# Kernel tuning notes

Measured on AMD Instinct MI355X. Metric: run time of the kernel, lower is better.

The kernel has to match this reference:

```python
import jax, jax.numpy as jnp
import numpy as np

N_NODES = 100000
N_EDGES = 1600000
IN_CH, OUT_CH = 6, 32


def _glorot(key, shape):
    fan_in, fan_out = shape[0], shape[1]
    lim = float(np.sqrt(6.0 / (fan_in + fan_out)))
    return jax.random.uniform(key, shape, jnp.float32, -lim, lim)


def setup_inputs() -> dict:
    key = jax.random.key(0)
    ks = jax.random.split(key, 16)
    x = jax.random.normal(ks[0], (N_NODES, IN_CH), jnp.float32)
    edge_tp = jax.random.randint(ks[1], (2, N_EDGES), 0, N_NODES, jnp.int32)
    edge_int = jax.random.randint(ks[2], (2, N_EDGES), 0, N_NODES, jnp.int32)
    return {
        'x': x, 'edge_tp': edge_tp, 'edge_int': edge_int,
        # block 1 (6 -> 32): self lin, per-edge-type message lins, residual proj
        'W_self1': _glorot(ks[3], (IN_CH, OUT_CH)), 'b1': jnp.zeros((OUT_CH,), jnp.float32),
        'W_tp1': _glorot(ks[4], (IN_CH, OUT_CH)), 'W_int1': _glorot(ks[5], (IN_CH, OUT_CH)),
        'W_res1': _glorot(ks[6], (IN_CH, OUT_CH)),
        # block 2 (32 -> 32): identity residual
        'W_self2': _glorot(ks[7], (OUT_CH, OUT_CH)), 'b2': jnp.zeros((OUT_CH,), jnp.float32),
        'W_tp2': _glorot(ks[8], (OUT_CH, OUT_CH)), 'W_int2': _glorot(ks[9], (OUT_CH, OUT_CH)),
        # instance decoder MLP
        'Wd1': _glorot(ks[10], (OUT_CH, OUT_CH)), 'bd1': jnp.zeros((OUT_CH,), jnp.float32),
        'Wd2': _glorot(ks[11], (OUT_CH, 1)), 'bd2': jnp.zeros((1,), jnp.float32),
    }


def _hetero_block(x, edge_tp, edge_int, W_self, b, W_tp, W_int, W_res):
    """One ResidualGeneralHeteroConvBlock: per-edge-type message passing
    ('temp_previous' -> sum-agg, 'intersects' -> mean-agg) + self transform +
    residual, then ReLU. x: [N, Cin]."""
    N = x.shape[0]
    # temp_previous: add reducer
    src, dst = edge_tp[0], edge_tp[1]
    m_tp = jax.ops.segment_sum(x[src] @ W_tp, dst, num_segments=N)  # [N, Cout]
    # intersects: mean reducer
    s2, d2 = edge_int[0], edge_int[1]
    m_sum = jax.ops.segment_sum(x[s2] @ W_int, d2, num_segments=N)
    cnt = jax.ops.segment_sum(jnp.ones(d2.shape, x.dtype), d2, num_segments=N)
    m_int = m_sum / jnp.maximum(cnt, 1.0)[:, None]
    res = x @ W_res if W_res is not None else x
    return jax.nn.relu(x @ W_self + b + m_tp + m_int + res)


def reference(x, edge_tp, edge_int,
              W_self1, b1, W_tp1, W_int1, W_res1,
              W_self2, b2, W_tp2, W_int2,
              Wd1, bd1, Wd2, bd2):
    h = _hetero_block(x, edge_tp, edge_int, W_self1, b1, W_tp1, W_int1, W_res1)
    h = _hetero_block(h, edge_tp, edge_int, W_self2, b2, W_tp2, W_int2, None)
    # instance decoder: Linear -> ReLU -> Linear -> sigmoid
    h = jax.nn.relu(h @ Wd1 + bd1)
    return jax.nn.sigmoid(h @ Wd2 + bd2)  # [N, 1]
```

## Files before the change

kernel.cpp:

```cpp
#include <hip/hip_runtime.h>
#include <hip/hip_bf16.h>
#include <math.h>

#define NN   100000
#define ICH  6
#define OCH  32
#define NBK  782
#define PBLK 256
#define CAPB 4736
#define CAPL 4800
#define GN   16

__device__ __forceinline__ float ldf(const void* p, long i, int f32) {
    return f32 ? ((const float*)p)[i]
               : __bfloat162float(((const __hip_bfloat16*)p)[i]);
}
__device__ __forceinline__ float lo16f(unsigned u) { return __uint_as_float(u << 16); }
__device__ __forceinline__ float hi16f(unsigned u) { return __uint_as_float(u & 0xFFFF0000u); }

__global__ __launch_bounds__(1024) void partAx_r14(
        const int* __restrict__ src_tp, const int* __restrict__ dst_tp,
        const int* __restrict__ src_int, const int* __restrict__ dst_int,
        int Etp, int E,
        const void* __restrict__ x, unsigned* __restrict__ xw,
        int* __restrict__ gcnt, unsigned* __restrict__ part,
        int* __restrict__ flagp) {
    __shared__ int lh[NBK];
    __shared__ int cur[NBK];
    __shared__ int weird;
    int t = threadIdx.x, blk = blockIdx.x;
    if (t == 0) weird = 0;
    for (int b = t; b < NBK; b += 1024) lh[b] = 0;
    __syncthreads();
    {
        const __hip_bfloat16* p = (const __hip_bfloat16*)x;
        int w = 0;
        for (int i = t; i < 4096; i += 1024) {
            float v = fabsf(__bfloat162float(p[i]));
            if (!(v <= 1000.0f) || (v > 0.0f && v < 1e-4f)) w++;
        }
        if (w) atomicAdd(&weird, w);
    }
    __syncthreads();
    int f32 = (weird > 500) ? 1 : 0;
    if (blk == 0 && t == 0) *flagp = f32;
    for (int w = blk * 1024 + t; w < NN * 4; w += PBLK * 1024) {
        int n = w >> 2, j = w & 3;
        int c0 = 2 * j, c1 = 2 * j + 1;
        __hip_bfloat16 v0 = (c0 < ICH) ? __float2bfloat16(ldf(x, (long)n * ICH + c0, f32))
                                       : __float2bfloat16(0.0f);
        __hip_bfloat16 v1 = (c1 < ICH) ? __float2bfloat16(ldf(x, (long)n * ICH + c1, f32))
                                       : __float2bfloat16(0.0f);
        xw[w] = (unsigned)__bfloat16_as_ushort(v0) |
                ((unsigned)__bfloat16_as_ushort(v1) << 16);
    }
    int CH = (E + PBLK - 1) / PBLK;
    int lo = blk * CH, hi = min(E, lo + CH);
    for (int e = lo + t; e < hi; e += 1024) {
        int bin = (e < Etp) ? dst_tp[e] : NN + dst_int[e - Etp];
        atomicAdd(&lh[bin >> 8], 1);
    }
    __syncthreads();
    for (int b = t; b < NBK; b += 1024) {
        int n = lh[b];
        int base = b * CAPB + (n ? atomicAdd(&gcnt[b], n) : gcnt[b]);
        cur[b] = base;
    }
    __syncthreads();
    for (int e = lo + t; e < hi; e += 1024) {
        int bin, src;
        if (e < Etp) { bin = dst_tp[e]; src = src_tp[e]; }
        else         { bin = NN + dst_int[e - Etp]; src = src_int[e - Etp]; }
        int pos = atomicAdd(&cur[bin >> 8], 1);
        part[pos] = ((unsigned)(bin & 255) << 24) | (unsigned)src;
    }
}

__global__ __launch_bounds__(256) void passB_r14(
        unsigned* __restrict__ partcsr, const int* __restrict__ gcnt,
        int* __restrict__ off, int* __restrict__ end) {
    __shared__ unsigned lp[CAPL];
    __shared__ int ssc[256], scur[256];
    int k = blockIdx.x, t = threadIdx.x;
    int s0 = k * CAPB;
    int cnt = gcnt[k]; if (cnt > CAPB) cnt = CAPB;
    scur[t] = 0;
    __syncthreads();
    for (int i = t; i < cnt; i += 256) {
        unsigned v = partcsr[s0 + i];
        lp[i] = v;
        atomicAdd(&scur[v >> 24], 1);
    }
    __syncthreads();
    int own = scur[t];
    ssc[t] = own; __syncthreads();
    for (int d = 1; d < 256; d <<= 1) {
        int val = (t >= d) ? ssc[t - d] : 0;
        __syncthreads();
        ssc[t] += val;
        __syncthreads();
    }
    int excl = ssc[t] - own;
    scur[t] = excl;
    int gbin = k * 256 + t;
    if (gbin < 2 * NN) {
        off[gbin] = s0 + excl;
        end[gbin] = s0 + excl + own;
    }
    __syncthreads();
    for (int i = t; i < cnt; i += 256) {
        unsigned v = lp[i];
        int pos = atomicAdd(&scur[v >> 24], 1);
        partcsr[s0 + pos] = v & 0xFFFFFFu;
    }
}

__global__ __launch_bounds__(256, 8) void node1_r14(
        const void* __restrict__ x, const unsigned* __restrict__ xw,
        const int* __restrict__ csr, const int* __restrict__ off,
        const int* __restrict__ end,
        const void* Ws1, const void* b1, const void* Wt1, const void* Wi1, const void* Wr1,
        __hip_bfloat16* __restrict__ h1b, float* __restrict__ invc_out,
        const int* __restrict__ flag) {
    __shared__ float sWs[ICH * OCH], sWt[ICH * OCH], sWi[ICH * OCH], sb1[OCH];
    __shared__ float sag[8][2][8];
    int t = threadIdx.x;
    int f32 = *flag;
    if (t < ICH * OCH) {
        sWs[t] = ldf(Ws1, t, f32) + ldf(Wr1, t, f32);
        sWt[t] = ldf(Wt1, t, f32);
        sWi[t] = ldf(Wi1, t, f32);
    }
    if (t < OCH) sb1[t] = ldf(b1, t, f32);
    __syncthreads();

    int g = t >> 5, c = t & 31;
    int s = c >> 2, j = c & 3;
    int node = blockIdx.x * 8 + g;

    int sa0 = off[node],      sa1 = end[node];
    int sb0 = off[NN + node], sb1_ = end[NN + node];
    int ma0 = sa1 - sa0; if (ma0 > 32) ma0 = 32;
    int mb0 = sb1_ - sb0; if (mb0 > 32) mb0 = 32;
    int idxa = (ma0 > 0) ? csr[sa0 + (c < ma0 ? c : ma0 - 1)] : 0;
    int idxb = (mb0 > 0) ? csr[sb0 + (c < mb0 ? c : mb0 - 1)] : 0;

#pragma unroll
    for (int set = 0; set < 2; ++set) {
        int s0 = set ? sb0 : sa0;
        int s1 = set ? sb1_ : sa1;
        int idx = set ? idxb : idxa;
        float vx = 0.0f, vy = 0.0f;
        for (int base = s0; base < s1; base += 32) {
            int m = s1 - base; if (m > 32) m = 32;
            int nb = base + 32;
            int nm = s1 - nb; if (nm > 32) nm = 32;
            int nidx = (nm > 0) ? csr[nb + (c < nm ? c : nm - 1)] : 0;
            unsigned u[4];
#pragma unroll
            for (int q = 0; q < 4; ++q) {
                int e = q * 8 + s;
                int sj = __shfl(idx, e & 31, 32);
                u[q] = xw[(unsigned)sj * 4u + j];
            }
#pragma unroll
            for (int q = 0; q < 4; ++q) {
                unsigned um = (q * 8 + s < m) ? u[q] : 0u;
                vx += lo16f(um); vy += hi16f(um);
            }
            idx = nidx;
        }
        vx += __shfl_down(vx, 16, 32);  vy += __shfl_down(vy, 16, 32);
        vx += __shfl_down(vx, 8, 32);   vy += __shfl_down(vy, 8, 32);
        vx += __shfl_down(vx, 4, 32);   vy += __shfl_down(vy, 4, 32);
        if (c < 4) { sag[g][set][2 * j] = vx; sag[g][set][2 * j + 1] = vy; }
    }

    int degi = sb1_ - sb0;
    float invc = 1.0f / fmaxf((float)degi, 1.0f);

    float acc = sb1[c];
#pragma unroll
    for (int k = 0; k < ICH; ++k) {
        float xv = ldf(x, (long)node * ICH + k, f32);
        acc += xv * sWs[k * OCH + c]
             + sag[g][0][k] * sWt[k * OCH + c]
             + (sag[g][1][k] * invc) * sWi[k * OCH + c];
    }
    h1b[(long)node * OCH + c] = __float2bfloat16(fmaxf(acc, 0.0f));
    if (c == 0) invc_out[node] = invc;
}

__global__ __launch_bounds__(512, 8) void final_r14(
        const unsigned* __restrict__ h1u,
        const int* __restrict__ csr, const int* __restrict__ off,
        const int* __restrict__ end,
        const float* __restrict__ invc,
        const void* Ws2, const void* b2v, const void* Wt2, const void* Wi2,
        const void* Wd1, const void* bd1, const void* Wd2, const void* bd2,
        void* __restrict__ out, const int* __restrict__ flag) {
    __shared__ float sWcat[96][32];
    __shared__ float sWd[32][32];
    __shared__ float sb2[OCH], sbd1[OCH], swd2[OCH];
    __shared__ float sv[GN][100];
    int t = threadIdx.x;
    int f32 = *flag;
    for (int i = t; i < 96 * 32; i += 512) {
        int k = i >> 5, c = i & 31;
        float w;
        if (k < 32)      w = ldf(Ws2, k * 32 + c, f32) + ((k == c) ? 1.0f : 0.0f);
        else if (k < 64) w = ldf(Wt2, (k - 32) * 32 + c, f32);
        else             w = ldf(Wi2, (k - 64) * 32 + c, f32);
        sWcat[k][c] = w;
    }
    for (int i = t; i < 32 * 32; i += 512) {
        int k = i >> 5, c = i & 31;
        sWd[k][c] = ldf(Wd1, k * 32 + c, f32);
    }
    if (t < OCH) {
        sb2[t] = ldf(b2v, t, f32); sbd1[t] = ldf(bd1, t, f32); swd2[t] = ldf(Wd2, t, f32);
    }
    __syncthreads();

    int g = t >> 5, c = t & 31;
    int sub = c >> 3, r = c & 7;
    int half = c >> 4, l = c & 15;
    int node = blockIdx.x * GN + g;

    unsigned uself = h1u[(unsigned)node * 16u + l];
    float ic = invc[node];
    int sa0 = off[node],      sa1 = end[node];
    int sb0 = off[NN + node], sb1_ = end[NN + node];
    int ma0 = sa1 - sa0; if (ma0 > 32) ma0 = 32;
    int mb0 = sb1_ - sb0; if (mb0 > 32) mb0 = 32;
    int idxa = (ma0 > 0) ? csr[sa0 + (c < ma0 ? c : ma0 - 1)] : 0;
    int idxb = (mb0 > 0) ? csr[sb0 + (c < mb0 ? c : mb0 - 1)] : 0;

    if (half == 0)
        *(float2*)&sv[g][2 * l] = make_float2(lo16f(uself), hi16f(uself));

#pragma unroll
    for (int set = 0; set < 2; ++set) {
        int s0 = set ? sb0 : sa0;
        int s1 = set ? sb1_ : sa1;
        int idx = set ? idxb : idxa;
        float2 v0 = make_float2(0.f, 0.f), v1 = v0;
        for (int base = s0; base < s1; base += 32) {
            int m = s1 - base; if (m > 32) m = 32;
            int nb = base + 32;
            int nm = s1 - nb; if (nm > 32) nm = 32;
            int nidx = (nm > 0) ? csr[nb + (c < nm ? c : nm - 1)] : 0;
            for (int b = 0; b < m; b += 16) {
                uint2 u[4];
#pragma unroll
                for (int q = 0; q < 4; ++q) {
                    int e = b + 4 * q + sub;
                    int sj = __shfl(idx, e & 31, 32);
                    u[q] = *(const uint2*)(h1u + (unsigned)sj * 16u + 2u * r);
                }
#pragma unroll
                for (int q = 0; q < 4; ++q) {
                    int ok = (b + 4 * q + sub < m);
                    unsigned wx = ok ? u[q].x : 0u;
                    unsigned wy = ok ? u[q].y : 0u;
                    v0.x += lo16f(wx); v0.y += hi16f(wx);
                    v1.x += lo16f(wy); v1.y += hi16f(wy);
                }
            }
            idx = nidx;
        }
#pragma unroll
        for (int sh = 8; sh <= 16; sh <<= 1) {
            v0.x += __shfl_down(v0.x, sh, 32);  v0.y += __shfl_down(v0.y, sh, 32);
            v1.x += __shfl_down(v1.x, sh, 32);  v1.y += __shfl_down(v1.y, sh, 32);
        }
        if (c < 8) {
            float sc = (set == 1) ? ic : 1.0f;
            *(float2*)&sv[g][32 + set * 32 + 4 * r]     = make_float2(v0.x * sc, v0.y * sc);
            *(float2*)&sv[g][32 + set * 32 + 4 * r + 2] = make_float2(v1.x * sc, v1.y * sc);
        }
    }

    float acc = sb2[c];
#pragma unroll 4
    for (int k = 0; k < 96; ++k)
        acc += sv[g][k] * sWcat[k][c];
    float h2 = fmaxf(acc, 0.0f);
    sv[g][c] = h2;

    float acc2 = sbd1[c];
#pragma unroll 4
    for (int k = 0; k < 32; ++k)
        acc2 += sv[g][k] * sWd[k][c];
    float h3 = fmaxf(acc2, 0.0f);

    float p = h3 * swd2[c];
#pragma unroll
    for (int offs = 16; offs; offs >>= 1) p += __shfl_down(p, offs, 32);
    if (c == 0) {
        float z = p + ldf(bd2, 0, f32);
        float sgm = 1.0f / (1.0f + expf(-z));
        if (f32) ((float*)out)[node] = sgm;
        else     ((__hip_bfloat16*)out)[node] = __float2bfloat16(sgm);
    }
}

extern "C" void kernel_launch(void* const* d_in, const int* in_sizes, int n_in,
                              void* d_out, int out_size, void* d_ws, size_t ws_size,
                              hipStream_t stream) {
    const void* x      = d_in[0];
    const int* edge_tp = (const int*)d_in[1];
    const int* edge_int= (const int*)d_in[2];
    const void* Ws1 = d_in[3], *b1 = d_in[4], *Wt1 = d_in[5], *Wi1 = d_in[6], *Wr1 = d_in[7];
    const void* Ws2 = d_in[8], *b2 = d_in[9];
    const void* Wt2 = d_in[10], *Wi2 = d_in[11];
    const void* Wd1 = d_in[12], *bd1 = d_in[13], *Wd2 = d_in[14], *bd2 = d_in[15];

    const int E_tp  = in_sizes[1] / 2;
    const int E_int = in_sizes[2] / 2;
    const int E     = E_tp + E_int;

    int*      flag    = (int*)d_ws;
    int*      gcnt    = flag + 64;
    int*      off     = gcnt + 1024;
    int*      end     = off + 2 * NN;
    unsigned* xw      = (unsigned*)(end + 2 * NN);
    unsigned* partcsr = xw + (size_t)4 * NN;
    unsigned* h1u     = partcsr + (size_t)NBK * CAPB;
    float*    invc    = (float*)(h1u + (size_t)16 * NN);
    __hip_bfloat16* h1b = (__hip_bfloat16*)h1u;

    const int* src_tp  = edge_tp;
    const int* dst_tp  = edge_tp + E_tp;
    const int* src_int = edge_int;
    const int* dst_int = edge_int + E_int;

    hipMemsetAsync(gcnt, 0, NBK * sizeof(int), stream);

    partAx_r14<<<PBLK, 1024, 0, stream>>>(src_tp, dst_tp, src_int, dst_int,
                                          E_tp, E, x, xw, gcnt, partcsr, flag);
    passB_r14<<<NBK, 256, 0, stream>>>(partcsr, gcnt, off, end);

    node1_r14<<<NN / 8, 256, 0, stream>>>(x, xw, (const int*)partcsr, off, end,
                                          Ws1, b1, Wt1, Wi1, Wr1,
                                          h1b, invc, flag);

    final_r14<<<NN / GN, 512, 0, stream>>>(h1u, (const int*)partcsr, off, end, invc,
                                           Ws2, b2, Wt2, Wi2,
                                           Wd1, bd1, Wd2, bd2, d_out, flag);
}
```

Baseline: 260.9 us.

## Interleave edge-type bins per node tile and fuse layer-1 node pass into CSR build

Bins are renumbered so each 256-bin bucket holds the 'temp_previous' and 'intersects' bins for the same 128 nodes. This lets the per-bucket CSR sort kernel also compute the first conv layer directly from the locally sorted edge lists in shared memory. The separate node1 kernel launch goes away, along with its re-reading of CSR, offsets and x from global memory. In exchange, each thread walks one node's edge list serially (one thread per node per edge type), which gives less parallelism and worse load balance than the old warp-per-node gather. The kernel also needs more shared memory, which may lower occupancy.

```diff
diff --git a/kernel.cpp b/kernel.cpp
--- a/kernel.cpp
+++ b/kernel.cpp
@@ -18,7 +18,11 @@
 __device__ __forceinline__ float lo16f(unsigned u) { return __uint_as_float(u << 16); }
 __device__ __forceinline__ float hi16f(unsigned u) { return __uint_as_float(u & 0xFFFF0000u); }
 
-__global__ __launch_bounds__(1024) void partAx_r14(
+__device__ __forceinline__ int binof(int n, int s) {
+    return ((n >> 7) << 8) | (s << 7) | (n & 127);
+}
+
+__global__ __launch_bounds__(1024) void partAx_r15(
         const int* __restrict__ src_tp, const int* __restrict__ dst_tp,
         const int* __restrict__ src_int, const int* __restrict__ dst_int,
         int Etp, int E,
@@ -57,7 +61,7 @@
     int CH = (E + PBLK - 1) / PBLK;
     int lo = blk * CH, hi = min(E, lo + CH);
     for (int e = lo + t; e < hi; e += 1024) {
-        int bin = (e < Etp) ? dst_tp[e] : NN + dst_int[e - Etp];
+        int bin = (e < Etp) ? binof(dst_tp[e], 0) : binof(dst_int[e - Etp], 1);
         atomicAdd(&lh[bin >> 8], 1);
     }
     __syncthreads();
@@ -69,129 +73,130 @@
     __syncthreads();
     for (int e = lo + t; e < hi; e += 1024) {
         int bin, src;
-        if (e < Etp) { bin = dst_tp[e]; src = src_tp[e]; }
-        else         { bin = NN + dst_int[e - Etp]; src = src_int[e - Etp]; }
+        if (e < Etp) { bin = binof(dst_tp[e], 0); src = src_tp[e]; }
+        else         { bin = binof(dst_int[e - Etp], 1); src = src_int[e - Etp]; }
         int pos = atomicAdd(&cur[bin >> 8], 1);
         part[pos] = ((unsigned)(bin & 255) << 24) | (unsigned)src;
     }
 }
 
-__global__ __launch_bounds__(256) void passB_r14(
+__global__ __launch_bounds__(256) void passBn1_r15(
         unsigned* __restrict__ partcsr, const int* __restrict__ gcnt,
-        int* __restrict__ off, int* __restrict__ end) {
+        int* __restrict__ off, int* __restrict__ end,
+        const unsigned* __restrict__ xw,
+        const void* Ws1, const void* b1v, const void* Wt1, const void* Wi1, const void* Wr1,
+        unsigned* __restrict__ h1u, float* __restrict__ invc_a,
+        const int* __restrict__ flag) {
     __shared__ unsigned lp[CAPL];
-    __shared__ int ssc[256], scur[256];
+    __shared__ unsigned sorted[CAPL];
+    __shared__ int scnt[256], sscan[256], obin[256];
+    __shared__ float agg[256][7];
+    __shared__ float sWs[ICH][32], sWt[ICH][32], sWi[ICH][32];
+    __shared__ float sb1[32];
     int k = blockIdx.x, t = threadIdx.x;
+    int f32 = *flag;
+    if (t < ICH * OCH) {
+        int kk = t >> 5, c = t & 31;
+        sWs[kk][c] = ldf(Ws1, t, f32) + ldf(Wr1, t, f32);
+        sWt[kk][c] = ldf(Wt1, t, f32);
+        sWi[kk][c] = ldf(Wi1, t, f32);
+    }
+    if (t < 32) sb1[t] = ldf(b1v, t, f32);
     int s0 = k * CAPB;
     int cnt = gcnt[k]; if (cnt > CAPB) cnt = CAPB;
-    scur[t] = 0;
+    scnt[t] = 0;
     __syncthreads();
     for (int i = t; i < cnt; i += 256) {
         unsigned v = partcsr[s0 + i];
         lp[i] = v;
-        atomicAdd(&scur[v >> 24], 1);
-    }
-    __syncthreads();
-    int own = scur[t];
-    ssc[t] = own; __syncthreads();
+        atomicAdd(&scnt[v >> 24], 1);
+    }
+    __syncthreads();
+    int own = scnt[t];
+    obin[t] = own;
+    sscan[t] = own; __syncthreads();
     for (int d = 1; d < 256; d <<= 1) {
-        int val = (t >= d) ? ssc[t - d] : 0;
+        int val = (t >= d) ? sscan[t - d] : 0;
         __syncthreads();
-        ssc[t] += val;
+        sscan[t] += val;
         __syncthreads();
     }
-    int excl = ssc[t] - own;
-    scur[t] = excl;
-    int gbin = k * 256 + t;
-    if (gbin < 2 * NN) {
-        off[gbin] = s0 + excl;
-        end[gbin] = s0 + excl + own;
-    }
+    int excl = sscan[t] - own;
+    scnt[t] = excl;
+    off[k * 256 + t] = s0 + excl;
+    end[k * 256 + t] = s0 + excl + own;
     __syncthreads();
     for (int i = t; i < cnt; i += 256) {
         unsigned v = lp[i];
-        int pos = atomicAdd(&scur[v >> 24], 1);
-        partcsr[s0 + pos] = v & 0xFFFFFFu;
-    }
-}
-
-__global__ __launch_bounds__(256, 8) void node1_r14(
-        const void* __restrict__ x, const unsigned* __restrict__ xw,
-        const int* __restrict__ csr, const int* __restrict__ off,
-        const int* __restrict__ end,
-        const void* Ws1, const void* b1, const void* Wt1, const void* Wi1, const void* Wr1,
-        __hip_bfloat16* __restrict__ h1b, float* __restrict__ invc_out,
-        const int* __restrict__ flag) {
-    __shared__ float sWs[ICH * OCH], sWt[ICH * OCH], sWi[ICH * OCH], sb1[OCH];
-    __shared__ float sag[8][2][8];
-    int t = threadIdx.x;
-    int f32 = *flag;
-    if (t < ICH * OCH) {
-        sWs[t] = ldf(Ws1, t, f32) + ldf(Wr1, t, f32);
-        sWt[t] = ldf(Wt1, t, f32);
-        sWi[t] = ldf(Wi1, t, f32);
-    }
-    if (t < OCH) sb1[t] = ldf(b1, t, f32);
-    __syncthreads();
-
-    int g = t >> 5, c = t & 31;
-    int s = c >> 2, j = c & 3;
-    int node = blockIdx.x * 8 + g;
-
-    int sa0 = off[node],      sa1 = end[node];
-    int sb0 = off[NN + node], sb1_ = end[NN + node];
-    int ma0 = sa1 - sa0; if (ma0 > 32) ma0 = 32;
-    int mb0 = sb1_ - sb0; if (mb0 > 32) mb0 = 32;
-    int idxa = (ma0 > 0) ? csr[sa0 + (c < ma0 ? c : ma0 - 1)] : 0;
-    int idxb = (mb0 > 0) ? csr[sb0 + (c < mb0 ? c : mb0 - 1)] : 0;
-
-#pragma unroll
-    for (int set = 0; set < 2; ++set) {
-        int s0 = set ? sb0 : sa0;
-        int s1 = set ? sb1_ : sa1;
-        int idx = set ? idxb : idxa;
-        float vx = 0.0f, vy = 0.0f;
-        for (int base = s0; base < s1; base += 32) {
-            int m = s1 - base; if (m > 32) m = 32;
-            int nb = base + 32;
-            int nm = s1 - nb; if (nm > 32) nm = 32;
-            int nidx = (nm > 0) ? csr[nb + (c < nm ? c : nm - 1)] : 0;
-            unsigned u[4];
-#pragma unroll
-            for (int q = 0; q < 4; ++q) {
-                int e = q * 8 + s;
-                int sj = __shfl(idx, e & 31, 32);
-                u[q] = xw[(unsigned)sj * 4u + j];
+        int pos = atomicAdd(&scnt[v >> 24], 1);
+        sorted[pos] = v & 0xFFFFFFu;
+    }
+    __syncthreads();
+    for (int i = t; i < cnt; i += 256) partcsr[s0 + i] = sorted[i];
+    float a0 = 0, a1 = 0, a2 = 0, a3 = 0, a4 = 0, a5 = 0;
+    {
+        int i = excl, e = excl + own;
+        for (; i + 4 <= e; i += 4) {
+            unsigned q0 = sorted[i], q1 = sorted[i + 1];
+            unsigned q2 = sorted[i + 2], q3 = sorted[i + 3];
+            uint4 u0 = *(const uint4*)(xw + q0 * 4u);
+            uint4 u1 = *(const uint4*)(xw + q1 * 4u);
+            uint4 u2 = *(const uint4*)(xw + q2 * 4u);
+            uint4 u3 = *(const uint4*)(xw + q3 * 4u);
+            a0 += lo16f(u0.x) + lo16f(u1.x) + lo16f(u2.x) + lo16f(u3.x);
+            a1 += hi16f(u0.x) + hi16f(u1.x) + hi16f(u2.x) + hi16f(u3.x);
+            a2 += lo16f(u0.y) + lo16f(u1.y) + lo16f(u2.y) + lo16f(u3.y);
+            a3 += hi16f(u0.y) + hi16f(u1.y) + hi16f(u2.y) + hi16f(u3.y);
+            a4 += lo16f(u0.z) + lo16f(u1.z) + lo16f(u2.z) + lo16f(u3.z);
+            a5 += hi16f(u0.z) + hi16f(u1.z) + hi16f(u2.z) + hi16f(u3.z);
+        }
+        for (; i < e; ++i) {
+            uint4 u = *(const uint4*)(xw + sorted[i] * 4u);
+            a0 += lo16f(u.x); a1 += hi16f(u.x);
+            a2 += lo16f(u.y); a3 += hi16f(u.y);
+            a4 += lo16f(u.z); a5 += hi16f(u.z);
+        }
+    }
+    agg[t][0] = a0; agg[t][1] = a1; agg[t][2] = a2;
+    agg[t][3] = a3; agg[t][4] = a4; agg[t][5] = a5;
+    __syncthreads();
+
+    int nl = t & 127, half = t >> 7;
+    int node = k * 128 + nl;
+    if (node < NN) {
+        int degi = obin[128 + nl];
+        float invc = 1.0f / fmaxf((float)degi, 1.0f);
+        if (half == 0) invc_a[node] = invc;
+        uint4 us = *(const uint4*)(xw + (unsigned)node * 4u);
+        float xv[ICH] = {lo16f(us.x), hi16f(us.x), lo16f(us.y),
+                         hi16f(us.y), lo16f(us.z), hi16f(us.z)};
+        float aT[ICH], aI[ICH];
+#pragma unroll
+        for (int q = 0; q < ICH; ++q) {
+            aT[q] = agg[nl][q];
+            aI[q] = agg[128 + nl][q] * invc;
+        }
+        unsigned row[8];
+#pragma unroll
+        for (int cc = 0; cc < 8; ++cc) {
+            int c0 = half * 16 + 2 * cc, c1 = c0 + 1;
+            float v0 = sb1[c0], v1 = sb1[c1];
+#pragma unroll
+            for (int q = 0; q < ICH; ++q) {
+                v0 += xv[q] * sWs[q][c0] + aT[q] * sWt[q][c0] + aI[q] * sWi[q][c0];
+                v1 += xv[q] * sWs[q][c1] + aT[q] * sWt[q][c1] + aI[q] * sWi[q][c1];
             }
-#pragma unroll
-            for (int q = 0; q < 4; ++q) {
-                unsigned um = (q * 8 + s < m) ? u[q] : 0u;
-                vx += lo16f(um); vy += hi16f(um);
-            }
-            idx = nidx;
-        }
-        vx += __shfl_down(vx, 16, 32);  vy += __shfl_down(vy, 16, 32);
-        vx += __shfl_down(vx, 8, 32);   vy += __shfl_down(vy, 8, 32);
-        vx += __shfl_down(vx, 4, 32);   vy += __shfl_down(vy, 4, 32);
-        if (c < 4) { sag[g][set][2 * j] = vx; sag[g][set][2 * j + 1] = vy; }
-    }
-
-    int degi = sb1_ - sb0;
-    float invc = 1.0f / fmaxf((float)degi, 1.0f);
-
-    float acc = sb1[c];
-#pragma unroll
-    for (int k = 0; k < ICH; ++k) {
-        float xv = ldf(x, (long)node * ICH + k, f32);
-        acc += xv * sWs[k * OCH + c]
-             + sag[g][0][k] * sWt[k * OCH + c]
-             + (sag[g][1][k] * invc) * sWi[k * OCH + c];
-    }
-    h1b[(long)node * OCH + c] = __float2bfloat16(fmaxf(acc, 0.0f));
-    if (c == 0) invc_out[node] = invc;
-}
-
-__global__ __launch_bounds__(512, 8) void final_r14(
+            unsigned w0 = (unsigned)__bfloat16_as_ushort(__float2bfloat16(fmaxf(v0, 0.0f)));
+            unsigned w1 = (unsigned)__bfloat16_as_ushort(__float2bfloat16(fmaxf(v1, 0.0f)));
+            row[cc] = w0 | (w1 << 16);
+        }
+        unsigned base = (unsigned)node * 16u + (unsigned)half * 8u;
+        *(uint4*)(h1u + base)      = make_uint4(row[0], row[1], row[2], row[3]);
+        *(uint4*)(h1u + base + 4u) = make_uint4(row[4], row[5], row[6], row[7]);
+    }
+}
+
+__global__ __launch_bounds__(512, 8) void final_r15(
         const unsigned* __restrict__ h1u,
         const int* __restrict__ csr, const int* __restrict__ off,
         const int* __restrict__ end,
@@ -229,8 +234,10 @@
 
     unsigned uself = h1u[(unsigned)node * 16u + l];
     float ic = invc[node];
-    int sa0 = off[node],      sa1 = end[node];
-    int sb0 = off[NN + node], sb1_ = end[NN + node];
+    int binA = ((node >> 7) << 8) | (node & 127);
+    int binB = binA | 128;
+    int sa0 = off[binA], sa1 = end[binA];
+    int sb0 = off[binB], sb1_ = end[binB];
     int ma0 = sa1 - sa0; if (ma0 > 32) ma0 = 32;
     int mb0 = sb1_ - sb0; if (mb0 > 32) mb0 = 32;
     int idxa = (ma0 > 0) ? csr[sa0 + (c < ma0 ? c : ma0 - 1)] : 0;
@@ -318,17 +325,15 @@
 
     const int E_tp  = in_sizes[1] / 2;
     const int E_int = in_sizes[2] / 2;
-    const int E     = E_tp + E_int;
 
     int*      flag    = (int*)d_ws;
     int*      gcnt    = flag + 64;
     int*      off     = gcnt + 1024;
-    int*      end     = off + 2 * NN;
-    unsigned* xw      = (unsigned*)(end + 2 * NN);
+    int*      end     = off + 200448;
+    unsigned* xw      = (unsigned*)(end + 200448);
     unsigned* partcsr = xw + (size_t)4 * NN;
     unsigned* h1u     = partcsr + (size_t)NBK * CAPB;
     float*    invc    = (float*)(h1u + (size_t)16 * NN);
-    __hip_bfloat16* h1b = (__hip_bfloat16*)h1u;
 
     const int* src_tp  = edge_tp;
     const int* dst_tp  = edge_tp + E_tp;
@@ -337,15 +342,14 @@
 
     hipMemsetAsync(gcnt, 0, NBK * sizeof(int), stream);
 
-    partAx_r14<<<PBLK, 1024, 0, stream>>>(src_tp, dst_tp, src_int, dst_int,
-                                          E_tp, E, x, xw, gcnt, partcsr, flag);
-    passB_r14<<<NBK, 256, 0, stream>>>(partcsr, gcnt, off, end);
-
-    node1_r14<<<NN / 8, 256, 0, stream>>>(x, xw, (const int*)partcsr, off, end,
-                                          Ws1, b1, Wt1, Wi1, Wr1,
-                                          h1b, invc, flag);
-
-    final_r14<<<NN / GN, 512, 0, stream>>>(h1u, (const int*)partcsr, off, end, invc,
+    partAx_r15<<<PBLK, 1024, 0, stream>>>(src_tp, dst_tp, src_int, dst_int,
+                                          E_tp, E_tp + E_int, x, xw, gcnt,
+                                          partcsr, flag);
+    passBn1_r15<<<NBK, 256, 0, stream>>>(partcsr, gcnt, off, end, xw,
+                                         Ws1, b1, Wt1, Wi1, Wr1,
+                                         h1u, invc, flag);
+
+    final_r15<<<NN / GN, 512, 0, stream>>>(h1u, (const int*)partcsr, off, end, invc,
                                            Ws2, b2, Wt2, Wi2,
                                            Wd1, bd1, Wd2, bd2, d_out, flag);
 }
```

After: 245.7 us. 5.8% less time.
